# Performance work log

Hardware: AMD Instinct MI355X
Metric: run time of the kernel (lower is better)

The kernel has to match this reference:

```python
import jax, jax.numpy as jnp
import numpy as np

N, D, K = 131072, 128, 512


def _sq_euclidean(x, c):
    x2 = jnp.sum(x * x, axis=1, keepdims=True)
    c2 = jnp.sum(c * c, axis=1)
    return x2 + c2 - 2.0 * (x @ c.T)


def setup_inputs() -> dict:
    key = jax.random.key(0)
    k1, k2 = jax.random.split(key)
    embedded = jax.random.normal(k1, (N, D), dtype=jnp.float32)
    centers = jax.random.normal(k2, (K, D), dtype=jnp.float32)
    count = jnp.ones((K,), dtype=jnp.int32) * 100  # as in fit()
    return {"embedded": embedded, "centers": centers, "count": count}


def reference(embedded, centers, count):
    dist = _sq_euclidean(embedded, centers)          # [N, K]
    loss = jnp.min(dist, axis=1).mean()              # dcn_loss
    labels = jnp.argmin(dist, axis=1)                # predict_hard

    # Sequential per-sample running-mean centroid update (Eq. 8):
    # count[c] += 1; eta = 1/count[c]; centers[c] = (1-eta)*centers[c] + eta*e
    def step(carry, inp):
        ctrs, cnt = carry
        e, c = inp
        new_cnt_c = cnt[c] + 1
        cnt = cnt.at[c].set(new_cnt_c)
        eta = 1.0 / new_cnt_c.astype(ctrs.dtype)
        ctrs = ctrs.at[c].set((1.0 - eta) * ctrs[c] + eta * e)
        return (ctrs, cnt), None

    (new_centers, new_count), _ = jax.lax.scan(step, (centers, count), (embedded, labels))
    return loss, labels, new_centers, new_count
```

## Files before the change

kernel.cpp:

```cpp
#include <hip/hip_runtime.h>

constexpr int NS = 131072;
constexpr int D  = 128;
constexpr int K  = 512;
constexpr int FLAG_CAP  = 65536;
constexpr int FLAG2_CAP = 32768;
constexpr float TAU1 = 0.05f;
constexpr float TAU2 = 2e-3f;
constexpr int SEG = 32;
constexpr int NB = 64;
constexpr int ITEMS = NS / NB;
constexpr float FIXSCALE = 1048576.0f;
constexpr double INVFIX  = 1.0 / 1048576.0;

using half8 = __attribute__((ext_vector_type(8))) _Float16;
using f32x4 = __attribute__((ext_vector_type(4))) float;


union H4 { short4 s4; _Float16 h[4]; };
union H8 { half8 v; _Float16 h[8]; };

__global__ void k_prep(const float* __restrict__ C, float* __restrict__ c2,
                       _Float16* __restrict__ Ch, _Float16* __restrict__ Cl) {
    int wave = (blockIdx.x * blockDim.x + threadIdx.x) >> 6;
    int lane = threadIdx.x & 63;
    const float* ck = C + (size_t)wave * D;
    float a = ck[lane], b = ck[lane + 64];
    _Float16 ha = (_Float16)a, hb = (_Float16)b;
    size_t o = (size_t)wave * D + lane;
    Ch[o] = ha;        Cl[o] = (_Float16)(a - (float)ha);
    Ch[o + 64] = hb;   Cl[o + 64] = (_Float16)(b - (float)hb);
    float s = fmaf(a, a, b * b);
    #pragma unroll
    for (int off = 32; off > 0; off >>= 1) s += __shfl_xor(s, off, 64);
    if (lane == 0) c2[wave] = s;
}

__global__ __launch_bounds__(256) void k_dist(
    const float* __restrict__ X, const _Float16* __restrict__ Ch,
    const float* __restrict__ c2,
    float* __restrict__ labF, float* __restrict__ mindist, int* __restrict__ labI,
    int* __restrict__ flags, int* __restrict__ flagCount)
{
    __shared__ _Float16 Cs[64][136];

    int tid = threadIdx.x;
    int wave = tid >> 6, lane = tid & 63;
    int l15 = lane & 15, lk = lane >> 4;
    int sbase = blockIdx.x * 64 + wave * 16;
    int srow = sbase + l15;

    half8 xa[4];
    const float* xp = X + (size_t)srow * D + lk * 8;
    #pragma unroll
    for (int kk = 0; kk < 4; ++kk) {
        float4 a = *(const float4*)(xp + kk * 32);
        float4 b = *(const float4*)(xp + kk * 32 + 4);
        H8 u;
        u.h[0] = (_Float16)a.x; u.h[1] = (_Float16)a.y;
        u.h[2] = (_Float16)a.z; u.h[3] = (_Float16)a.w;
        u.h[4] = (_Float16)b.x; u.h[5] = (_Float16)b.y;
        u.h[6] = (_Float16)b.z; u.h[7] = (_Float16)b.w;
        xa[kk] = u.v;
    }

    float m1[4], m2[4]; int ag[4];
    #pragma unroll
    for (int r = 0; r < 4; ++r) { m1[r] = 3.4e38f; m2[r] = 3.4e38f; ag[r] = 0; }

    int crow = tid >> 2, cpart = tid & 3;
    for (int chunk = 0; chunk < 8; ++chunk) {
        const int4* src = (const int4*)(Ch + (size_t)(chunk * 64 + crow) * D + cpart * 32);
        int4 v0 = src[0], v1 = src[1], v2 = src[2], v3 = src[3];
        *(int4*)&Cs[crow][cpart * 32]      = v0;
        *(int4*)&Cs[crow][cpart * 32 + 8]  = v1;
        *(int4*)&Cs[crow][cpart * 32 + 16] = v2;
        *(int4*)&Cs[crow][cpart * 32 + 24] = v3;
        __syncthreads();

        #pragma unroll
        for (int t = 0; t < 4; ++t) {
            int cl = t * 16 + l15;
            int ci = chunk * 64 + cl;
            half8 b0 = *(const half8*)&Cs[cl][lk * 8];
            half8 b1 = *(const half8*)&Cs[cl][lk * 8 + 32];
            half8 b2 = *(const half8*)&Cs[cl][lk * 8 + 64];
            half8 b3 = *(const half8*)&Cs[cl][lk * 8 + 96];
            float cc = c2[ci];
            f32x4 acc = (f32x4){0.f, 0.f, 0.f, 0.f};
            acc = __builtin_amdgcn_mfma_f32_16x16x32_f16(xa[0], b0, acc, 0, 0, 0);
            acc = __builtin_amdgcn_mfma_f32_16x16x32_f16(xa[1], b1, acc, 0, 0, 0);
            acc = __builtin_amdgcn_mfma_f32_16x16x32_f16(xa[2], b2, acc, 0, 0, 0);
            acc = __builtin_amdgcn_mfma_f32_16x16x32_f16(xa[3], b3, acc, 0, 0, 0);
            #pragma unroll
            for (int r = 0; r < 4; ++r) {
                float s = fmaf(-2.f, acc[r], cc);
                bool b = s < m1[r];
                m2[r] = b ? m1[r] : fminf(m2[r], s);
                m1[r] = b ? s : m1[r];
                ag[r] = b ? ci : ag[r];
            }
        }
        __syncthreads();
    }

    #pragma unroll
    for (int off = 1; off <= 8; off <<= 1)
        #pragma unroll
        for (int r = 0; r < 4; ++r) {
            float o1 = __shfl_xor(m1[r], off, 64);
            float o2 = __shfl_xor(m2[r], off, 64);
            int   oa = __shfl_xor(ag[r], off, 64);
            bool b = (o1 < m1[r]) || (o1 == m1[r] && oa < ag[r]);
            float lo1 = b ? o1 : m1[r];
            float hi1 = b ? m1[r] : o1;
            m2[r] = fminf(fminf(m2[r], o2), hi1);
            m1[r] = lo1;
            ag[r] = b ? oa : ag[r];
        }

    if (l15 == 0) {
        #pragma unroll
        for (int r = 0; r < 4; ++r) {
            int i = sbase + lk * 4 + r;
            labF[i] = (float)ag[r];
            labI[i] = ag[r];
            mindist[i] = m1[r];
            if (m2[r] - m1[r] < TAU1) {
                int p = atomicAdd(flagCount, 1);
                if (p < FLAG_CAP) flags[p] = i;
            }
        }
    }
}

__global__ __launch_bounds__(256, 2) void k_mid(
    const float* __restrict__ X, const _Float16* __restrict__ Ch,
    const _Float16* __restrict__ Cl, const float* __restrict__ c2,
    const int* __restrict__ flagCount, const int* __restrict__ flags,
    float* __restrict__ labF, float* __restrict__ mindist, int* __restrict__ labI,
    int* __restrict__ flags2, int* __restrict__ flagCount2)
{
    __shared__ _Float16 Ah[64][136];
    __shared__ _Float16 Al[64][136];
    __shared__ float red1[4][64];
    __shared__ float red2[4][64];
    __shared__ int   reda[4][64];
    __shared__ int   sidx[64];

    int nf = *flagCount;
    if (nf > FLAG_CAP) nf = FLAG_CAP;
    int ntile = (nf + 63) >> 6;
    int tid = threadIdx.x;
    int wave = tid >> 6, lane = tid & 63;
    int l15 = lane & 15, lk = lane >> 4;

    for (int t = blockIdx.x; t < ntile; t += gridDim.x) {
        if (tid < 64) {
            int p = t * 64 + tid;
            sidx[tid] = flags[p < nf ? p : nf - 1];
        }
        __syncthreads();
        {
            int row = tid >> 2, part = tid & 3;
            const float4* src = (const float4*)(X + (size_t)sidx[row] * D + part * 32);
            #pragma unroll
            for (int j = 0; j < 8; ++j) {
                float4 v = src[j];
                H4 uh, ul;
                uh.h[0] = (_Float16)v.x; ul.h[0] = (_Float16)(v.x - (float)uh.h[0]);
                uh.h[1] = (_Float16)v.y; ul.h[1] = (_Float16)(v.y - (float)uh.h[1]);
                uh.h[2] = (_Float16)v.z; ul.h[2] = (_Float16)(v.z - (float)uh.h[2]);
                uh.h[3] = (_Float16)v.w; ul.h[3] = (_Float16)(v.w - (float)uh.h[3]);
                *(short4*)&Ah[row][part * 32 + j * 4] = uh.s4;
                *(short4*)&Al[row][part * 32 + j * 4] = ul.s4;
            }
        }
        __syncthreads();

        float m1[4], m2[4]; int ag[4];
        #pragma unroll
        for (int n = 0; n < 4; ++n) { m1[n] = 3.4e38f; m2[n] = 3.4e38f; ag[n] = 0; }

        for (int chunk = 0; chunk < 8; ++chunk) {
            int cb = chunk * 64 + wave * 16;
            const half8* pch = (const half8*)(Ch + (size_t)(cb + l15) * D + lk * 8);
            const half8* pcl = (const half8*)(Cl + (size_t)(cb + l15) * D + lk * 8);
            half8 ah[4], al[4];
            #pragma unroll
            for (int kk = 0; kk < 4; ++kk) { ah[kk] = pch[kk * 4]; al[kk] = pcl[kk * 4]; }
            f32x4 acc[4];
            #pragma unroll
            for (int n = 0; n < 4; ++n) acc[n] = (f32x4){0.f, 0.f, 0.f, 0.f};
            #pragma unroll
            for (int kk = 0; kk < 4; ++kk) {
                half8 xh[4], xl[4];
                #pragma unroll
                for (int n = 0; n < 4; ++n) {
                    xh[n] = *(const half8*)&Ah[n * 16 + l15][kk * 32 + lk * 8];
                    xl[n] = *(const half8*)&Al[n * 16 + l15][kk * 32 + lk * 8];
                }
                #pragma unroll
                for (int n = 0; n < 4; ++n)
                    acc[n] = __builtin_amdgcn_mfma_f32_16x16x32_f16(ah[kk], xh[n], acc[n], 0, 0, 0);
                #pragma unroll
                for (int n = 0; n < 4; ++n)
                    acc[n] = __builtin_amdgcn_mfma_f32_16x16x32_f16(al[kk], xh[n], acc[n], 0, 0, 0);
                #pragma unroll
                for (int n = 0; n < 4; ++n)
                    acc[n] = __builtin_amdgcn_mfma_f32_16x16x32_f16(ah[kk], xl[n], acc[n], 0, 0, 0);
            }
            float cc[4];
            #pragma unroll
            for (int r = 0; r < 4; ++r) cc[r] = c2[cb + lk * 4 + r];
            #pragma unroll
            for (int n = 0; n < 4; ++n)
                #pragma unroll
                for (int r = 0; r < 4; ++r) {
                    float s = fmaf(-2.f, acc[n][r], cc[r]);
                    int ci = cb + lk * 4 + r;
                    bool b = s < m1[n];
                    m2[n] = b ? m1[n] : fminf(m2[n], s);
                    m1[n] = b ? s : m1[n];
                    ag[n] = b ? ci : ag[n];
                }
        }

        #pragma unroll
        for (int off = 16; off <= 32; off <<= 1)
            #pragma unroll
            for (int n = 0; n < 4; ++n) {
                float o1 = __shfl_xor(m1[n], off, 64);
                float o2 = __shfl_xor(m2[n], off, 64);
                int   oa = __shfl_xor(ag[n], off, 64);
                bool b = (o1 < m1[n]) || (o1 == m1[n] && oa < ag[n]);
                float lo1 = b ? o1 : m1[n];
                float hi1 = b ? m1[n] : o1;
                m2[n] = fminf(fminf(m2[n], o2), hi1);
                m1[n] = lo1;
                ag[n] = b ? oa : ag[n];
            }
        if (lane < 16) {
            #pragma unroll
            for (int n = 0; n < 4; ++n) {
                red1[wave][n * 16 + l15] = m1[n];
                red2[wave][n * 16 + l15] = m2[n];
                reda[wave][n * 16 + l15] = ag[n];
            }
        }
        __syncthreads();

        if (tid < 64) {
            float M1 = red1[0][tid], M2 = red2[0][tid]; int A = reda[0][tid];
            #pragma unroll
            for (int w = 1; w < 4; ++w) {
                float o1 = red1[w][tid], o2 = red2[w][tid]; int oa = reda[w][tid];
                bool b = (o1 < M1) || (o1 == M1 && oa < A);
                float lo1 = b ? o1 : M1;
                float hi1 = b ? M1 : o1;
                M2 = fminf(fminf(M2, o2), hi1);
                M1 = lo1;
                A = b ? oa : A;
            }
            int i = sidx[tid];
            labF[i] = (float)A;
            labI[i] = A;
            mindist[i] = M1;
            bool fl = (M2 - M1 < TAU2);
            unsigned long long mask = __ballot(fl);
            int nfl = (int)__popcll(mask);
            int base = 0;
            if (tid == 0 && nfl) base = atomicAdd(flagCount2, nfl);
            base = __shfl(base, 0, 64);
            if (fl) {
                int pos = base + (int)__popcll(mask & ((1ull << tid) - 1ull));
                if (pos < FLAG2_CAP) flags2[pos] = i;
            }
        }
        __syncthreads();
    }
}

__global__ void k_refine(const float* __restrict__ X, const float* __restrict__ C,
                         const int* __restrict__ flagCount2, const int* __restrict__ flags2,
                         float* __restrict__ labF, float* __restrict__ mindist,
                         int* __restrict__ labI)
{
    int nf = *flagCount2;
    if (nf > FLAG2_CAP) nf = FLAG2_CAP;
    int lane = threadIdx.x;
    for (int f = blockIdx.x; f < nf; f += gridDim.x) {
        int i = flags2[f];
        const float* xr = X + (size_t)i * D;
        double best = 1e300;
        int bestk = K;
        for (int k = lane; k < K; k += 64) {
            const float* ck = C + (size_t)k * D;
            double dot = 0.0, cc = 0.0;
            for (int d = 0; d < D; ++d) {
                double cd = (double)ck[d];
                dot = fma((double)xr[d], cd, dot);
                cc  = fma(cd, cd, cc);
            }
            double s = cc - 2.0 * dot;
            if (s < best) { best = s; bestk = k; }
        }
        #pragma unroll
        for (int off = 32; off > 0; off >>= 1) {
            double ob = __shfl_xor(best, off, 64);
            int okk   = __shfl_xor(bestk, off, 64);
            if (ob < best || (ob == best && okk < bestk)) { best = ob; bestk = okk; }
        }
        if (lane == 0) {
            labF[i] = (float)bestk;
            labI[i] = bestk;
            mindist[i] = (float)best;
        }
    }
}

__global__ __launch_bounds__(256) void k_bhl(const int* __restrict__ labI,
                                             const float* __restrict__ mindist,
                                             int* __restrict__ H,
                                             double* __restrict__ lossSum) {
    __shared__ int h[K];
    __shared__ double shd[4];
    for (int c = threadIdx.x; c < K; c += 256) h[c] = 0;
    __syncthreads();
    int base = blockIdx.x * ITEMS;
    double s = 0.0;
    #pragma unroll
    for (int it = 0; it < ITEMS / 256; ++it) {
        int i = base + it * 256 + threadIdx.x;
        atomicAdd(&h[labI[i]], 1);
        s += (double)mindist[i];
    }
    __syncthreads();
    for (int c = threadIdx.x; c < K; c += 256) H[blockIdx.x * K + c] = h[c];
    #pragma unroll
    for (int off = 32; off > 0; off >>= 1) s += __shfl_xor(s, off, 64);
    int wid = threadIdx.x >> 6, lane = threadIdx.x & 63;
    if (lane == 0) shd[wid] = s;
    __syncthreads();
    if (threadIdx.x == 0)
        atomicAdd(lossSum, (shd[0] + shd[1]) + (shd[2] + shd[3]));
}

__global__ void k_sc(int* __restrict__ H, int* __restrict__ counts) {
    __shared__ int sh[K];
    int c = threadIdx.x;
    int run = 0;
    for (int b = 0; b < NB; ++b) { int t = H[b * K + c]; H[b * K + c] = run; run += t; }
    counts[c] = run;
    sh[c] = run;
    __syncthreads();
    int my = run;
    for (int off = 1; off < K; off <<= 1) {
        int v = (c >= off) ? sh[c - off] : 0;
        __syncthreads();
        sh[c] += v;
        __syncthreads();
    }
    int excl = sh[c] - my;
    for (int b = 0; b < NB; ++b) H[b * K + c] += excl;
}

__global__ __launch_bounds__(256) void k_scatter2(const int* __restrict__ labI,
                                                  const int* __restrict__ H,
                                                  int* __restrict__ bucket) {
    __shared__ int cur[K];
    for (int c = threadIdx.x; c < K; c += 256) cur[c] = H[blockIdx.x * K + c];
    __syncthreads();
    int base = blockIdx.x * ITEMS;
    #pragma unroll
    for (int it = 0; it < ITEMS / 256; ++it) {
        int i = base + it * 256 + threadIdx.x;
        int pos = atomicAdd(&cur[labI[i]], 1);
        bucket[pos] = i;
    }
}

__global__ __launch_bounds__(128) void k_sumseg(
    const float* __restrict__ X, const int* __restrict__ labI,
    const int* __restrict__ bucket, unsigned long long* __restrict__ acc,
    double* __restrict__ x2Sum)
{
    int d = threadIdx.x;
    int beg = blockIdx.x * SEG;
    long long s = 0;
    double s2 = 0.0;
    int prev = -1;
    for (int j = beg; j < beg + SEG; ++j) {
        int idx = bucket[j];
        int lab = labI[idx];
        if (lab != prev) {
            if (prev >= 0) atomicAdd(&acc[(size_t)prev * D + d], (unsigned long long)s);
            s = 0; prev = lab;
        }
        float v = X[(size_t)idx * D + d];
        s += (long long)__float2int_rn(v * FIXSCALE);
        s2 = fma((double)v, (double)v, s2);
    }
    if (prev >= 0) atomicAdd(&acc[(size_t)prev * D + d], (unsigned long long)s);
    #pragma unroll
    for (int off = 32; off > 0; off >>= 1) s2 += __shfl_xor(s2, off, 64);
    __shared__ double shx[2];
    int wid = d >> 6;
    if ((d & 63) == 0) shx[wid] = s2;
    __syncthreads();
    if (d == 0) atomicAdd(&x2Sum[blockIdx.x & 7], shx[0] + shx[1]);
}

__global__ void k_avg(const float* __restrict__ C, const int* __restrict__ cnt,
                      const int* __restrict__ counts,
                      const unsigned long long* __restrict__ acc,
                      float* __restrict__ outC, float* __restrict__ outCnt,
                      const double* __restrict__ lossSum,
                      const double* __restrict__ x2Sum, float* __restrict__ outLoss)
{
    int t = blockIdx.x * blockDim.x + threadIdx.x;
    int c = t >> 7, d = t & 127;
    double s = (double)(long long)acc[t] * INVFIX;
    int m = counts[c], n0 = cnt[c];
    double nm = (double)(n0 + m);
    outC[t] = (float)(((double)n0 * (double)C[t] + s) / nm);
    if (d == 0) outCnt[c] = (float)(n0 + m);
    if (t == 0) {
        double x2 = 0.0;
        #pragma unroll
        for (int j = 0; j < 8; ++j) x2 += x2Sum[j];
        outLoss[0] = (float)((*lossSum + x2) / (double)NS);
    }
}

extern "C" void kernel_launch(void* const* d_in, const int* in_sizes, int n_in,
                              void* d_out, int out_size, void* d_ws, size_t ws_size,
                              hipStream_t stream)
{
    const float* X  = (const float*)d_in[0];
    const float* C  = (const float*)d_in[1];
    const int* cnt  = (const int*)d_in[2];

    float* out     = (float*)d_out;
    float* outLoss = out;
    float* outLab  = out + 1;
    float* outCen  = out + 1 + NS;
    float* outCnt  = out + 1 + NS + (size_t)K * D;

    char* ws = (char*)d_ws;
    double* lossSum = (double*)(ws + 0);
    double* x2Sum   = (double*)(ws + 8);
    int* flagCount  = (int*)(ws + 72);
    int* flagCount2 = (int*)(ws + 76);
    float* c2       = (float*)(ws + 80);
    int* counts     = (int*)(ws + 2128);
    float* mindist  = (float*)(ws + 4176);
    int* labI       = (int*)(ws + 528464);
    int* flags      = (int*)(ws + 1052752);
    int* flags2     = (int*)(ws + 1314896);
    int* H          = (int*)(ws + 1445968);
    int* bucket     = (int*)(ws + 1577040);
    unsigned long long* acc = (unsigned long long*)(ws + 2101328);
    _Float16* Ch    = (_Float16*)(ws + 2625616);
    _Float16* Cl    = (_Float16*)(ws + 2756688);

    hipMemsetAsync(d_ws, 0, 80, stream);
    hipMemsetAsync(ws + 2101328, 0, (size_t)K * D * 8, stream);
    k_prep<<<K / 4, 256, 0, stream>>>(C, c2, Ch, Cl);
    k_dist<<<NS / 64, 256, 0, stream>>>(X, Ch, c2, outLab, mindist, labI, flags, flagCount);
    k_mid<<<512, 256, 0, stream>>>(X, Ch, Cl, c2, flagCount, flags,
                                   outLab, mindist, labI, flags2, flagCount2);
    k_refine<<<2048, 64, 0, stream>>>(X, C, flagCount2, flags2, outLab, mindist, labI);
    k_bhl<<<NB, 256, 0, stream>>>(labI, mindist, H, lossSum);
    k_sc<<<1, K, 0, stream>>>(H, counts);
    k_scatter2<<<NB, 256, 0, stream>>>(labI, H, bucket);
    k_sumseg<<<NS / SEG, 128, 0, stream>>>(X, labI, bucket, acc, x2Sum);
    k_avg<<<K * D / 256, 256, 0, stream>>>(C, cnt, counts, acc, outCen, outCnt,
                                           lossSum, x2Sum, outLoss);
}
```

Measured before the change: 200.7 us.

## Process 32 rows per wave in k_dist to reuse center tiles across two MFMA groups

Each wave now handles two 16-row sample tiles, so every B fragment read from shared memory feeds two MFMA chains, and the grid is halved. The block stages center norms in shared memory instead of reading them from global memory per tile. The second-min update is rewritten as min(m2, max(m1, s)), which saves a select. The cost is more registers per thread and fewer blocks, which may lower occupancy.

```diff
diff --git a/kernel.cpp b/kernel.cpp
--- a/kernel.cpp
+++ b/kernel.cpp
@@ -43,30 +43,51 @@
     int* __restrict__ flags, int* __restrict__ flagCount)
 {
     __shared__ _Float16 Cs[64][136];
+    __shared__ float sC2[K];
 
     int tid = threadIdx.x;
     int wave = tid >> 6, lane = tid & 63;
     int l15 = lane & 15, lk = lane >> 4;
-    int sbase = blockIdx.x * 64 + wave * 16;
-    int srow = sbase + l15;
-
-    half8 xa[4];
-    const float* xp = X + (size_t)srow * D + lk * 8;
-    #pragma unroll
-    for (int kk = 0; kk < 4; ++kk) {
-        float4 a = *(const float4*)(xp + kk * 32);
-        float4 b = *(const float4*)(xp + kk * 32 + 4);
-        H8 u;
-        u.h[0] = (_Float16)a.x; u.h[1] = (_Float16)a.y;
-        u.h[2] = (_Float16)a.z; u.h[3] = (_Float16)a.w;
-        u.h[4] = (_Float16)b.x; u.h[5] = (_Float16)b.y;
-        u.h[6] = (_Float16)b.z; u.h[7] = (_Float16)b.w;
-        xa[kk] = u.v;
-    }
-
-    float m1[4], m2[4]; int ag[4];
-    #pragma unroll
-    for (int r = 0; r < 4; ++r) { m1[r] = 3.4e38f; m2[r] = 3.4e38f; ag[r] = 0; }
+    int sbase = blockIdx.x * 128 + wave * 32;
+
+    sC2[tid] = c2[tid];
+    sC2[tid + 256] = c2[tid + 256];
+
+    half8 xa0[4], xa1[4];
+    {
+        const float* xp0 = X + (size_t)(sbase + l15) * D + lk * 8;
+        const float* xp1 = X + (size_t)(sbase + 16 + l15) * D + lk * 8;
+        #pragma unroll
+        for (int kk = 0; kk < 4; ++kk) {
+            float4 a = *(const float4*)(xp0 + kk * 32);
+            float4 b = *(const float4*)(xp0 + kk * 32 + 4);
+            H8 u;
+            u.h[0] = (_Float16)a.x; u.h[1] = (_Float16)a.y;
+            u.h[2] = (_Float16)a.z; u.h[3] = (_Float16)a.w;
+            u.h[4] = (_Float16)b.x; u.h[5] = (_Float16)b.y;
+            u.h[6] = (_Float16)b.z; u.h[7] = (_Float16)b.w;
+            xa0[kk] = u.v;
+        }
+        #pragma unroll
+        for (int kk = 0; kk < 4; ++kk) {
+            float4 a = *(const float4*)(xp1 + kk * 32);
+            float4 b = *(const float4*)(xp1 + kk * 32 + 4);
+            H8 u;
+            u.h[0] = (_Float16)a.x; u.h[1] = (_Float16)a.y;
+            u.h[2] = (_Float16)a.z; u.h[3] = (_Float16)a.w;
+            u.h[4] = (_Float16)b.x; u.h[5] = (_Float16)b.y;
+            u.h[6] = (_Float16)b.z; u.h[7] = (_Float16)b.w;
+            xa1[kk] = u.v;
+        }
+    }
+
+    float m1a[4], m2a[4], m1b[4], m2b[4];
+    int aga[4], agb[4];
+    #pragma unroll
+    for (int r = 0; r < 4; ++r) {
+        m1a[r] = 3.4e38f; m2a[r] = 3.4e38f; aga[r] = 0;
+        m1b[r] = 3.4e38f; m2b[r] = 3.4e38f; agb[r] = 0;
+    }
 
     int crow = tid >> 2, cpart = tid & 3;
     for (int chunk = 0; chunk < 8; ++chunk) {
@@ -86,47 +107,84 @@
             half8 b1 = *(const half8*)&Cs[cl][lk * 8 + 32];
             half8 b2 = *(const half8*)&Cs[cl][lk * 8 + 64];
             half8 b3 = *(const half8*)&Cs[cl][lk * 8 + 96];
-            float cc = c2[ci];
+            float cc = sC2[ci];
             f32x4 acc = (f32x4){0.f, 0.f, 0.f, 0.f};
-            acc = __builtin_amdgcn_mfma_f32_16x16x32_f16(xa[0], b0, acc, 0, 0, 0);
-            acc = __builtin_amdgcn_mfma_f32_16x16x32_f16(xa[1], b1, acc, 0, 0, 0);
-            acc = __builtin_amdgcn_mfma_f32_16x16x32_f16(xa[2], b2, acc, 0, 0, 0);
-            acc = __builtin_amdgcn_mfma_f32_16x16x32_f16(xa[3], b3, acc, 0, 0, 0);
+            acc = __builtin_amdgcn_mfma_f32_16x16x32_f16(xa0[0], b0, acc, 0, 0, 0);
+            acc = __builtin_amdgcn_mfma_f32_16x16x32_f16(xa0[1], b1, acc, 0, 0, 0);
+            acc = __builtin_amdgcn_mfma_f32_16x16x32_f16(xa0[2], b2, acc, 0, 0, 0);
+            acc = __builtin_amdgcn_mfma_f32_16x16x32_f16(xa0[3], b3, acc, 0, 0, 0);
             #pragma unroll
             for (int r = 0; r < 4; ++r) {
                 float s = fmaf(-2.f, acc[r], cc);
-                bool b = s < m1[r];
-                m2[r] = b ? m1[r] : fminf(m2[r], s);
-                m1[r] = b ? s : m1[r];
-                ag[r] = b ? ci : ag[r];
-            }
-        }
-        __syncthreads();
-    }
-
-    #pragma unroll
-    for (int off = 1; off <= 8; off <<= 1)
+                bool b = s < m1a[r];
+                m2a[r] = fminf(m2a[r], fmaxf(m1a[r], s));
+                m1a[r] = b ? s : m1a[r];
+                aga[r] = b ? ci : aga[r];
+            }
+            acc = (f32x4){0.f, 0.f, 0.f, 0.f};
+            acc = __builtin_amdgcn_mfma_f32_16x16x32_f16(xa1[0], b0, acc, 0, 0, 0);
+            acc = __builtin_amdgcn_mfma_f32_16x16x32_f16(xa1[1], b1, acc, 0, 0, 0);
+            acc = __builtin_amdgcn_mfma_f32_16x16x32_f16(xa1[2], b2, acc, 0, 0, 0);
+            acc = __builtin_amdgcn_mfma_f32_16x16x32_f16(xa1[3], b3, acc, 0, 0, 0);
+            #pragma unroll
+            for (int r = 0; r < 4; ++r) {
+                float s = fmaf(-2.f, acc[r], cc);
+                bool b = s < m1b[r];
+                m2b[r] = fminf(m2b[r], fmaxf(m1b[r], s));
+                m1b[r] = b ? s : m1b[r];
+                agb[r] = b ? ci : agb[r];
+            }
+        }
+        __syncthreads();
+    }
+
+    #pragma unroll
+    for (int off = 1; off <= 8; off <<= 1) {
         #pragma unroll
         for (int r = 0; r < 4; ++r) {
-            float o1 = __shfl_xor(m1[r], off, 64);
-            float o2 = __shfl_xor(m2[r], off, 64);
-            int   oa = __shfl_xor(ag[r], off, 64);
-            bool b = (o1 < m1[r]) || (o1 == m1[r] && oa < ag[r]);
-            float lo1 = b ? o1 : m1[r];
-            float hi1 = b ? m1[r] : o1;
-            m2[r] = fminf(fminf(m2[r], o2), hi1);
-            m1[r] = lo1;
-            ag[r] = b ? oa : ag[r];
-        }
+            float o1 = __shfl_xor(m1a[r], off, 64);
+            float o2 = __shfl_xor(m2a[r], off, 64);
+            int   oa = __shfl_xor(aga[r], off, 64);
+            bool b = (o1 < m1a[r]) || (o1 == m1a[r] && oa < aga[r]);
+            float lo1 = b ? o1 : m1a[r];
+            float hi1 = b ? m1a[r] : o1;
+            m2a[r] = fminf(fminf(m2a[r], o2), hi1);
+            m1a[r] = lo1;
+            aga[r] = b ? oa : aga[r];
+        }
+        #pragma unroll
+        for (int r = 0; r < 4; ++r) {
+            float o1 = __shfl_xor(m1b[r], off, 64);
+            float o2 = __shfl_xor(m2b[r], off, 64);
+            int   oa = __shfl_xor(agb[r], off, 64);
+            bool b = (o1 < m1b[r]) || (o1 == m1b[r] && oa < agb[r]);
+            float lo1 = b ? o1 : m1b[r];
+            float hi1 = b ? m1b[r] : o1;
+            m2b[r] = fminf(fminf(m2b[r], o2), hi1);
+            m1b[r] = lo1;
+            agb[r] = b ? oa : agb[r];
+        }
+    }
 
     if (l15 == 0) {
         #pragma unroll
         for (int r = 0; r < 4; ++r) {
             int i = sbase + lk * 4 + r;
-            labF[i] = (float)ag[r];
-            labI[i] = ag[r];
-            mindist[i] = m1[r];
-            if (m2[r] - m1[r] < TAU1) {
+            labF[i] = (float)aga[r];
+            labI[i] = aga[r];
+            mindist[i] = m1a[r];
+            if (m2a[r] - m1a[r] < TAU1) {
+                int p = atomicAdd(flagCount, 1);
+                if (p < FLAG_CAP) flags[p] = i;
+            }
+        }
+        #pragma unroll
+        for (int r = 0; r < 4; ++r) {
+            int i = sbase + 16 + lk * 4 + r;
+            labF[i] = (float)agb[r];
+            labI[i] = agb[r];
+            mindist[i] = m1b[r];
+            if (m2b[r] - m1b[r] < TAU1) {
                 int p = atomicAdd(flagCount, 1);
                 if (p < FLAG_CAP) flags[p] = i;
             }
@@ -467,7 +525,7 @@
     hipMemsetAsync(d_ws, 0, 80, stream);
     hipMemsetAsync(ws + 2101328, 0, (size_t)K * D * 8, stream);
     k_prep<<<K / 4, 256, 0, stream>>>(C, c2, Ch, Cl);
-    k_dist<<<NS / 64, 256, 0, stream>>>(X, Ch, c2, outLab, mindist, labI, flags, flagCount);
+    k_dist<<<NS / 128, 256, 0, stream>>>(X, Ch, c2, outLab, mindist, labI, flags, flagCount);
     k_mid<<<512, 256, 0, stream>>>(X, Ch, Cl, c2, flagCount, flags,
                                    outLab, mindist, labI, flags2, flagCount2);
     k_refine<<<2048, 64, 0, stream>>>(X, C, flagCount2, flags2, outLab, mindist, labI);
```

New measurement: 171.8 us. 14.4% less time.
